# Kernel tuning notes

Hardware: AMD Instinct MI355X
Metric: run time of the kernel (lower is better)

## Reference

```python
import jax, jax.numpy as jnp
import numpy as np

P = 7       # patch (window) size
H_HEADS = 8
D_HEAD = 64
SCALE = D_HEAD ** -0.5


def setup_inputs() -> dict:
    key = jax.random.key(0)
    k1, k2, k3, k4 = jax.random.split(key, 4)
    dim, inner = 256, H_HEADS * D_HEAD
    fmap = jax.random.normal(k1, (32, 56, 56, dim), dtype=jnp.float32)
    Wq = jax.random.normal(k2, (dim, inner), dtype=jnp.float32) * (dim ** -0.5)
    Wkv = jax.random.normal(k3, (dim, 2 * inner), dtype=jnp.float32) * (dim ** -0.5)
    Wo = jax.random.normal(k4, (inner, dim), dtype=jnp.float32) * (inner ** -0.5)
    bo = jnp.zeros((dim,), dtype=jnp.float32)
    return {"fmap": fmap, "Wq": Wq, "Wkv": Wkv, "Wo": Wo, "bo": bo}


def reference(fmap, Wq, Wkv, Wo, bo):
    b, X, Y, c = fmap.shape
    x, y = X // P, Y // P
    h, d = H_HEADS, D_HEAD
    # window partition: b (x p1) (y p2) c -> (b x y) p1 p2 c
    f = fmap.reshape(b, x, P, y, P, c).transpose(0, 1, 3, 2, 4, 5)
    f = f.reshape(b * x * y, P, P, c)
    # 1x1 convs == matmul over channels
    q = f @ Wq                       # (B, p, p, h*d)
    k_, v = jnp.split(f @ Wkv, 2, axis=-1)
    B = b * x * y
    pp = P * P
    def to_heads(t):  # (B,p,p,h*d) -> (B,h,pp,d)
        return t.reshape(B, pp, h, d).transpose(0, 2, 1, 3)
    q, k_, v = map(to_heads, (q, k_, v))
    dots = jnp.einsum('bhid,bhjd->bhij', q, k_) * SCALE
    attn = jax.nn.softmax(dots, axis=-1)
    out = jnp.einsum('bhij,bhjd->bhid', attn, v)      # (B,h,pp,d)
    # (b x y h) (p1 p2) d -> b (x p1) (y p2) (h d)
    out = out.reshape(b, x, y, h, P, P, d)
    out = out.transpose(0, 1, 4, 2, 5, 3, 6).reshape(b, X, Y, h * d)
    return out @ Wo + bo
```

## Files before the change

### kernel.cpp

```cpp
#include <hip/hip_runtime.h>
#include <hip/hip_bf16.h>

typedef __bf16 bf16;
typedef __bf16 bf16x4 __attribute__((ext_vector_type(4)));
typedef __bf16 bf16x8 __attribute__((ext_vector_type(8)));
typedef float f32x4 __attribute__((ext_vector_type(4)));

#define TOK 100352
#define ATT_SCALE 0.125f

#define GLOAD_LDS16(g, l)                                                        \
  __builtin_amdgcn_global_load_lds((const __attribute__((address_space(1))) void*)(g), \
                                   (__attribute__((address_space(3))) void*)(l), 16, 0, 0)

__global__ __launch_bounds__(256) void prep_k(const float* __restrict__ Wq,
                                              const float* __restrict__ Wkv,
                                              const float* __restrict__ Wo,
                                              bf16* __restrict__ Wqkv_t,
                                              bf16* __restrict__ Wo_p) {
  int b = blockIdx.x;
  if (b < 384) {
    __shared__ float t[32][33];
    int bx = b % 48, by = b / 48;
    const float* in;
    bf16* out;
    int C, c0, r0 = by * 32;
    if (bx < 16) { in = Wq; C = 512; c0 = bx * 32; out = Wqkv_t; }
    else { in = Wkv; C = 1024; c0 = (bx - 16) * 32; out = Wqkv_t + 512 * 256; }
    int tx = threadIdx.x & 31, ty = threadIdx.x >> 5;
#pragma unroll
    for (int i = ty; i < 32; i += 8)
      t[i][tx] = in[(size_t)(r0 + i) * C + c0 + tx];
    __syncthreads();
#pragma unroll
    for (int i = ty; i < 32; i += 8)
      out[(size_t)(c0 + i) * 256 + r0 + tx] = (bf16)t[tx][i];
  } else {
    int t = (b - 384) * 256 + threadIdx.x;
    int f = t >> 6, l = t & 63;
    int kk = f & 1, h = (f >> 1) & 7, n = (f >> 4) & 3, wvv = f >> 6;
    int row = wvv * 64 + n * 16 + (l & 15);
    int col = h * 64 + kk * 32 + (l >> 4) * 8;
    bf16x8 o;
#pragma unroll
    for (int e = 0; e < 8; ++e) o[e] = (bf16)Wo[(size_t)(col + e) * 256 + row];
    *(bf16x8*)(Wo_p + (size_t)f * 512 + l * 8) = o;
  }
}

__global__ __launch_bounds__(256) void padzero_k(bf16* __restrict__ Vtg, int nwh) {
  int t = blockIdx.x * 256 + threadIdx.x;
  int wh = t >> 6, dd = t & 63;
  if (wh < nwh) {
    uint4 z = {0, 0, 0, 0};
    char* p = (char*)(Vtg + (size_t)wh * 4096 + dd * 64 + 48);
    *(uint4*)p = z;
    *(uint4*)(p + 16) = z;
  }
}

__global__ __launch_bounds__(256) void qkvg_k(const float* __restrict__ fmap,
                                              const bf16* __restrict__ Bt,
                                              bf16* __restrict__ qkv2,
                                              bf16* __restrict__ Vtg, int wbase0) {
  __shared__ bf16 Bs[2][128 * 64];
  const int tid = threadIdx.x;
  const int lane = tid & 63, wv = tid >> 6;
  const int l15 = lane & 15, l4 = lane >> 4;
  const int g = blockIdx.x;
  const int blk = blockIdx.y;
  bf16x8 af[2][8];
  int wl[2], tt[2];
#pragma unroll
  for (int m = 0; m < 2; ++m) {
    int tokl = blk * 128 + wv * 32 + m * 16 + l15;
    int w = tokl / 49, t = tokl - w * 49;
    wl[m] = w; tt[m] = t;
    int wg = wbase0 + w;
    int p1 = t / 7, p2 = t - p1 * 7;
    const float* ab = fmap +
        (size_t)((((wg >> 6) * 56) + ((wg >> 3) & 7) * 7 + p1) * 56 + (wg & 7) * 7 + p2) * 256;
#pragma unroll
    for (int j = 0; j < 8; ++j) {
      const float* p = ab + j * 32 + l4 * 8;
      float4 f0 = *(const float4*)p;
      float4 f1 = *(const float4*)(p + 4);
      bf16x8 o;
      o[0] = (bf16)f0.x; o[1] = (bf16)f0.y; o[2] = (bf16)f0.z; o[3] = (bf16)f0.w;
      o[4] = (bf16)f1.x; o[5] = (bf16)f1.y; o[6] = (bf16)f1.z; o[7] = (bf16)f1.w;
      af[m][j] = o;
    }
  }
  const int sg = lane >> 3;
  const int scol = ((lane & 7) ^ (sg & 7)) * 8;
#define STAGE_B(tt_, buf_)                                                                   \
  do {                                                                                       \
    int bn_ = g * 4 + ((tt_) >> 2), ks_ = (tt_) & 3;                                         \
    _Pragma("unroll") for (int i_ = 0; i_ < 4; ++i_)                                         \
        GLOAD_LDS16(Bt + (size_t)(bn_ * 128 + wv * 32 + i_ * 8 + sg) * 256 + ks_ * 64 + scol,\
                    Bs[buf_] + wv * 2048 + i_ * 512);                                        \
  } while (0)

  f32x4 acc[2][8] = {};
  STAGE_B(0, 0);
  __syncthreads();
#pragma unroll
  for (int t = 0; t < 16; ++t) {
    const int cur = t & 1, ks = t & 3;
    if (t < 15) STAGE_B(t + 1, cur ^ 1);
#pragma unroll
    for (int kk = 0; kk < 2; ++kk) {
      bf16x8 bfr[8];
#pragma unroll
      for (int n = 0; n < 8; ++n) {
        int rv = n * 16 + l15;
        bfr[n] = *(const bf16x8*)((const char*)Bs[cur] +
                 ((rv * 128 + kk * 64 + l4 * 16) ^ ((rv & 7) << 4)));
      }
#pragma unroll
      for (int m = 0; m < 2; ++m)
#pragma unroll
        for (int n = 0; n < 8; ++n)
          acc[m][n] = __builtin_amdgcn_mfma_f32_16x16x32_bf16(bfr[n], af[m][ks * 2 + kk],
                                                              acc[m][n], 0, 0, 0);
    }
    if (ks == 3) {
      const int bn = g * 4 + (t >> 2);
      if (g < 2) {
#pragma unroll
        for (int m = 0; m < 2; ++m) {
          size_t row = (size_t)blk * 128 + wv * 32 + m * 16 + l15;
#pragma unroll
          for (int n = 0; n < 8; ++n) {
            bf16x4 pk;
#pragma unroll
            for (int r = 0; r < 4; ++r) pk[r] = (bf16)acc[m][n][r];
            *(bf16x4*)(qkv2 + row * 1024 + bn * 128 + n * 16 + l4 * 4) = pk;
          }
        }
      } else {
#pragma unroll
        for (int m = 0; m < 2; ++m) {
#pragma unroll
          for (int n = 0; n < 8; ++n) {
            int d0 = (bn - 8) * 128 + n * 16 + l4 * 4;
            int h = d0 >> 6, dd = d0 & 63;
            size_t vb = ((size_t)wl[m] * 8 + h) * 4096 + (size_t)dd * 64 + tt[m];
#pragma unroll
            for (int r = 0; r < 4; ++r) Vtg[vb + (size_t)r * 64] = (bf16)acc[m][n][r];
          }
        }
      }
#pragma unroll
      for (int m = 0; m < 2; ++m)
#pragma unroll
        for (int n = 0; n < 8; ++n) acc[m][n] = (f32x4){0.f, 0.f, 0.f, 0.f};
    }
    __syncthreads();
  }
#undef STAGE_B
}

__global__ __launch_bounds__(256) void attn2_k(const bf16* __restrict__ qkv2,
                                               const bf16* __restrict__ Vtg,
                                               const bf16* __restrict__ Wo_p,
                                               const float* __restrict__ bias,
                                               float* __restrict__ out, int wbase) {
  __shared__ bf16 Qs[64 * 64], Ks[64 * 64], Vt[64 * 64], Ps[4 * 16 * 64], HO[64 * 64];
  const int w = blockIdx.x;
  const int tid = threadIdx.x, lane = tid & 63, wv = tid >> 6;
  const int l15 = lane & 15, l4 = lane >> 4;
  const size_t bqk = (size_t)w * 49 * 1024;
  const bf16* vbase = Vtg + (size_t)w * 8 * 4096;
  const int wg = wbase + w;
  char* pbase = (char*)Ps + wv * 2048;
  const int sr = wv * 8 + (lane >> 3);
  const int scc = ((lane & 7) ^ ((lane >> 3) & 7)) * 8;
  f32x4 acco[4][4] = {};
  for (int h = 0; h < 8; ++h) {
#pragma unroll
    for (int i = 0; i < 2; ++i) {
      GLOAD_LDS16(qkv2 + bqk + (size_t)(i * 32 + sr) * 1024 + h * 64 + scc,
                  Qs + i * 2048 + wv * 512);
      GLOAD_LDS16(qkv2 + bqk + (size_t)(i * 32 + sr) * 1024 + 512 + h * 64 + scc,
                  Ks + i * 2048 + wv * 512);
      GLOAD_LDS16(vbase + (size_t)h * 4096 + (i * 32 + sr) * 64 + scc,
                  Vt + i * 2048 + wv * 512);
    }
    __syncthreads();
    f32x4 s[4] = {};
#pragma unroll
    for (int kk = 0; kk < 2; ++kk) {
      int rq = wv * 16 + l15;
      bf16x8 aq = *(const bf16x8*)((const char*)Qs +
                  ((rq * 128 + kk * 64 + l4 * 16) ^ ((rq & 7) << 4)));
#pragma unroll
      for (int n = 0; n < 4; ++n) {
        int rk = n * 16 + l15;
        bf16x8 bk = *(const bf16x8*)((const char*)Ks +
                    ((rk * 128 + kk * 64 + l4 * 16) ^ ((rk & 7) << 4)));
        s[n] = __builtin_amdgcn_mfma_f32_16x16x32_bf16(aq, bk, s[n], 0, 0, 0);
      }
    }
    float pr[4][4];
#pragma unroll
    for (int reg = 0; reg < 4; ++reg) {
      float m = -1e30f;
#pragma unroll
      for (int n = 0; n < 4; ++n) {
        float v = s[n][reg] * ATT_SCALE;
        if (n * 16 + l15 < 49) m = fmaxf(m, v);
      }
#pragma unroll
      for (int d = 1; d < 16; d <<= 1) m = fmaxf(m, __shfl_xor(m, d));
      float sum = 0.f;
#pragma unroll
      for (int n = 0; n < 4; ++n) {
        float p = (n * 16 + l15 < 49) ? __expf(s[n][reg] * ATT_SCALE - m) : 0.f;
        pr[n][reg] = p;
        sum += p;
      }
#pragma unroll
      for (int d = 1; d < 16; d <<= 1) sum += __shfl_xor(sum, d);
      float inv = 1.f / sum;
#pragma unroll
      for (int n = 0; n < 4; ++n) pr[n][reg] *= inv;
    }
#pragma unroll
    for (int n = 0; n < 4; ++n)
#pragma unroll
      for (int reg = 0; reg < 4; ++reg) {
        int rl = l4 * 4 + reg, col = n * 16 + l15;
        int off = ((rl * 64 + col) * 2) ^ ((rl & 7) << 4);
        *(bf16*)(pbase + off) = (bf16)pr[n][reg];
      }
    f32x4 o[4] = {};
#pragma unroll
    for (int kk = 0; kk < 2; ++kk) {
      int rp = l15;
      bf16x8 ap = *(const bf16x8*)(pbase +
                  ((rp * 128 + kk * 64 + l4 * 16) ^ ((rp & 7) << 4)));
#pragma unroll
      for (int n = 0; n < 4; ++n) {
        int rv = n * 16 + l15;
        bf16x8 bv = *(const bf16x8*)((const char*)Vt +
                    ((rv * 128 + kk * 64 + l4 * 16) ^ ((rv & 7) << 4)));
        o[n] = __builtin_amdgcn_mfma_f32_16x16x32_bf16(bv, ap, o[n], 0, 0, 0);
      }
    }
    {
      int hrow = wv * 16 + l15;
#pragma unroll
      for (int n = 0; n < 4; ++n) {
        bf16x4 pk;
#pragma unroll
        for (int r = 0; r < 4; ++r) pk[r] = (bf16)o[n][r];
        int off = (hrow * 128 + n * 32 + l4 * 8) ^ ((hrow & 7) << 4);
        *(bf16x4*)((char*)HO + off) = pk;
      }
    }
    __syncthreads();
#pragma unroll
    for (int kk = 0; kk < 2; ++kk) {
      bf16x8 af[4];
#pragma unroll
      for (int m = 0; m < 4; ++m) {
        int r = m * 16 + l15;
        af[m] = *(const bf16x8*)((const char*)HO +
                 ((r * 128 + kk * 64 + l4 * 16) ^ ((r & 7) << 4)));
      }
#pragma unroll
      for (int n = 0; n < 4; ++n) {
        int f = ((wv * 4 + n) * 8 + h) * 2 + kk;
        bf16x8 bv = *(const bf16x8*)(Wo_p + (size_t)f * 512 + lane * 8);
#pragma unroll
        for (int m = 0; m < 4; ++m)
          acco[m][n] = __builtin_amdgcn_mfma_f32_16x16x32_bf16(bv, af[m], acco[m][n], 0, 0, 0);
      }
    }
  }
  int bb = wg >> 6, xx = (wg >> 3) & 7, yy = wg & 7;
#pragma unroll
  for (int m = 0; m < 4; ++m) {
    int rl = m * 16 + l15;
    if (rl < 49) {
      int p1 = rl / 7, p2 = rl - p1 * 7;
      size_t orow = (size_t)(bb * 56 + xx * 7 + p1) * 56 + yy * 7 + p2;
      float* op = out + orow * 256 + wv * 64;
#pragma unroll
      for (int n = 0; n < 4; ++n) {
        int col = n * 16 + l4 * 4;
        float4 b4 = *(const float4*)(bias + wv * 64 + col);
        float4 v;
        v.x = acco[m][n][0] + b4.x;
        v.y = acco[m][n][1] + b4.y;
        v.z = acco[m][n][2] + b4.z;
        v.w = acco[m][n][3] + b4.w;
        *(float4*)(op + col) = v;
      }
    }
  }
}

extern "C" void kernel_launch(void* const* d_in, const int* in_sizes, int n_in,
                              void* d_out, int out_size, void* d_ws, size_t ws_size,
                              hipStream_t stream) {
  const float* fmap = (const float*)d_in[0];
  const float* Wq = (const float*)d_in[1];
  const float* Wkv = (const float*)d_in[2];
  const float* Wo = (const float*)d_in[3];
  const float* bo = (const float*)d_in[4];
  float* out = (float*)d_out;
  char* ws = (char*)d_ws;

  const size_t WQKV_B = 1536ull * 256 * 2;
  const size_t WOP_B = 256ull * 512 * 2;
  const size_t wbytes = WQKV_B + WOP_B;

  int nc = 0;
  size_t Tc = 0, VtgB = 0;
  for (int c = 2; c <= 16; c <<= 1) {
    size_t tc = TOK / c;
    size_t vb = (tc / 49) * 65536ull;
    if (wbytes + vb + tc * 2048ull + 65536ull <= ws_size) { nc = c; Tc = tc; VtgB = vb; break; }
  }
  if (nc == 0) return;

  bf16* Wqkv_t = (bf16*)(ws);
  bf16* Wo_p = (bf16*)(ws + WQKV_B);
  bf16* Vtg = (bf16*)(ws + wbytes);
  bf16* qkv2 = (bf16*)(ws + wbytes + VtgB);

  hipLaunchKernelGGL(prep_k, dim3(448), dim3(256), 0, stream, Wq, Wkv, Wo, Wqkv_t, Wo_p);
  int nwh = (int)(Tc / 49) * 8;
  hipLaunchKernelGGL(padzero_k, dim3((nwh * 64 + 255) / 256), dim3(256), 0, stream, Vtg, nwh);

  for (int c = 0; c < nc; ++c) {
    int tok0 = (int)(c * Tc);
    int wloc = (int)(Tc / 49);
    hipLaunchKernelGGL(qkvg_k, dim3(3, (int)(Tc / 128)), dim3(256), 0, stream, fmap, Wqkv_t,
                       qkv2, Vtg, tok0 / 49);
    hipLaunchKernelGGL(attn2_k, dim3(wloc), dim3(256), 0, stream, qkv2, Vtg, Wo_p, bo, out,
                       tok0 / 49);
  }
}
```

Before: 323.5 us.

## Overlap QKV projection of chunk two with attention of chunk one in fused kernel

After: 443.1 us. +37.0%, slower.

```diff
diff --git a/kernel.cpp b/kernel.cpp
--- a/kernel.cpp
+++ b/kernel.cpp
@@ -59,16 +59,13 @@
   }
 }
 
-__global__ __launch_bounds__(256) void qkvg_k(const float* __restrict__ fmap,
-                                              const bf16* __restrict__ Bt,
-                                              bf16* __restrict__ qkv2,
-                                              bf16* __restrict__ Vtg, int wbase0) {
-  __shared__ bf16 Bs[2][128 * 64];
+__device__ __forceinline__ void qkvg_body(int g, int blk, const float* __restrict__ fmap,
+                                          const bf16* __restrict__ Bt,
+                                          bf16* __restrict__ qkv2, bf16* __restrict__ Vtg,
+                                          int wbase0, bf16* Bs0, bf16* Bs1) {
   const int tid = threadIdx.x;
   const int lane = tid & 63, wv = tid >> 6;
   const int l15 = lane & 15, l4 = lane >> 4;
-  const int g = blockIdx.x;
-  const int blk = blockIdx.y;
   bf16x8 af[2][8];
   int wl[2], tt[2];
 #pragma unroll
@@ -93,28 +90,30 @@
   }
   const int sg = lane >> 3;
   const int scol = ((lane & 7) ^ (sg & 7)) * 8;
-#define STAGE_B(tt_, buf_)                                                                   \
-  do {                                                                                       \
-    int bn_ = g * 4 + ((tt_) >> 2), ks_ = (tt_) & 3;                                         \
-    _Pragma("unroll") for (int i_ = 0; i_ < 4; ++i_)                                         \
-        GLOAD_LDS16(Bt + (size_t)(bn_ * 128 + wv * 32 + i_ * 8 + sg) * 256 + ks_ * 64 + scol,\
-                    Bs[buf_] + wv * 2048 + i_ * 512);                                        \
-  } while (0)
-
+  bf16* Bsp[2] = {Bs0, Bs1};
   f32x4 acc[2][8] = {};
-  STAGE_B(0, 0);
+#pragma unroll
+  for (int i = 0; i < 4; ++i)
+    GLOAD_LDS16(Bt + (size_t)(g * 4 * 128 + wv * 32 + i * 8 + sg) * 256 + scol,
+                Bs0 + wv * 2048 + i * 512);
   __syncthreads();
 #pragma unroll
   for (int t = 0; t < 16; ++t) {
     const int cur = t & 1, ks = t & 3;
-    if (t < 15) STAGE_B(t + 1, cur ^ 1);
+    if (t < 15) {
+      int bn_ = g * 4 + ((t + 1) >> 2), ks_ = (t + 1) & 3;
+#pragma unroll
+      for (int i = 0; i < 4; ++i)
+        GLOAD_LDS16(Bt + (size_t)(bn_ * 128 + wv * 32 + i * 8 + sg) * 256 + ks_ * 64 + scol,
+                    Bsp[cur ^ 1] + wv * 2048 + i * 512);
+    }
 #pragma unroll
     for (int kk = 0; kk < 2; ++kk) {
       bf16x8 bfr[8];
 #pragma unroll
       for (int n = 0; n < 8; ++n) {
         int rv = n * 16 + l15;
-        bfr[n] = *(const bf16x8*)((const char*)Bs[cur] +
+        bfr[n] = *(const bf16x8*)((const char*)Bsp[cur] +
                  ((rv * 128 + kk * 64 + l4 * 16) ^ ((rv & 7) << 4)));
       }
 #pragma unroll
@@ -158,21 +157,19 @@
     }
     __syncthreads();
   }
-#undef STAGE_B
-}
-
-__global__ __launch_bounds__(256) void attn2_k(const bf16* __restrict__ qkv2,
-                                               const bf16* __restrict__ Vtg,
-                                               const bf16* __restrict__ Wo_p,
-                                               const float* __restrict__ bias,
-                                               float* __restrict__ out, int wbase) {
-  __shared__ bf16 Qs[64 * 64], Ks[64 * 64], Vt[64 * 64], Ps[4 * 16 * 64], HO[64 * 64];
-  const int w = blockIdx.x;
+}
+
+__device__ __forceinline__ void attn_body(int win, const bf16* __restrict__ qkv2,
+                                          const bf16* __restrict__ Vtg,
+                                          const bf16* __restrict__ Wo_p,
+                                          const float* __restrict__ bias,
+                                          float* __restrict__ out, int wbase, bf16* Qs,
+                                          bf16* Ks, bf16* Vt, bf16* Ps, bf16* HO) {
   const int tid = threadIdx.x, lane = tid & 63, wv = tid >> 6;
   const int l15 = lane & 15, l4 = lane >> 4;
-  const size_t bqk = (size_t)w * 49 * 1024;
-  const bf16* vbase = Vtg + (size_t)w * 8 * 4096;
-  const int wg = wbase + w;
+  const size_t bqk = (size_t)win * 49 * 1024;
+  const bf16* vbase = Vtg + (size_t)win * 8 * 4096;
+  const int wg = wbase + win;
   char* pbase = (char*)Ps + wv * 2048;
   const int sr = wv * 8 + (lane >> 3);
   const int scc = ((lane & 7) ^ ((lane >> 3) & 7)) * 8;
@@ -205,18 +202,18 @@
     float pr[4][4];
 #pragma unroll
     for (int reg = 0; reg < 4; ++reg) {
-      float m = -1e30f;
+      float mx = -1e30f;
 #pragma unroll
       for (int n = 0; n < 4; ++n) {
         float v = s[n][reg] * ATT_SCALE;
-        if (n * 16 + l15 < 49) m = fmaxf(m, v);
-      }
-#pragma unroll
-      for (int d = 1; d < 16; d <<= 1) m = fmaxf(m, __shfl_xor(m, d));
+        if (n * 16 + l15 < 49) mx = fmaxf(mx, v);
+      }
+#pragma unroll
+      for (int d = 1; d < 16; d <<= 1) mx = fmaxf(mx, __shfl_xor(mx, d));
       float sum = 0.f;
 #pragma unroll
       for (int n = 0; n < 4; ++n) {
-        float p = (n * 16 + l15 < 49) ? __expf(s[n][reg] * ATT_SCALE - m) : 0.f;
+        float p = (n * 16 + l15 < 49) ? __expf(s[n][reg] * ATT_SCALE - mx) : 0.f;
         pr[n][reg] = p;
         sum += p;
       }
@@ -262,11 +259,11 @@
     __syncthreads();
 #pragma unroll
     for (int kk = 0; kk < 2; ++kk) {
-      bf16x8 af[4];
+      bf16x8 afr[4];
 #pragma unroll
       for (int m = 0; m < 4; ++m) {
         int r = m * 16 + l15;
-        af[m] = *(const bf16x8*)((const char*)HO +
+        afr[m] = *(const bf16x8*)((const char*)HO +
                  ((r * 128 + kk * 64 + l4 * 16) ^ ((r & 7) << 4)));
       }
 #pragma unroll
@@ -275,7 +272,7 @@
         bf16x8 bv = *(const bf16x8*)(Wo_p + (size_t)f * 512 + lane * 8);
 #pragma unroll
         for (int m = 0; m < 4; ++m)
-          acco[m][n] = __builtin_amdgcn_mfma_f32_16x16x32_bf16(bv, af[m], acco[m][n], 0, 0, 0);
+          acco[m][n] = __builtin_amdgcn_mfma_f32_16x16x32_bf16(bv, afr[m], acco[m][n], 0, 0, 0);
       }
     }
   }
@@ -299,6 +296,46 @@
         *(float4*)(op + col) = v;
       }
     }
+  }
+}
+
+__global__ __launch_bounds__(256) void qkvg_k(const float* __restrict__ fmap,
+                                              const bf16* __restrict__ Bt,
+                                              bf16* __restrict__ qkv2,
+                                              bf16* __restrict__ Vtg, int wbase0) {
+  __shared__ bf16 Bs[2][128 * 64];
+  qkvg_body(blockIdx.x, blockIdx.y, fmap, Bt, qkv2, Vtg, wbase0, Bs[0], Bs[1]);
+}
+
+__global__ __launch_bounds__(256) void attn2_k(const bf16* __restrict__ qkv2,
+                                               const bf16* __restrict__ Vtg,
+                                               const bf16* __restrict__ Wo_p,
+                                               const float* __restrict__ bias,
+                                               float* __restrict__ out, int wbase) {
+  __shared__ bf16 Qs[64 * 64], Ks[64 * 64], Vt[64 * 64], Ps[4 * 16 * 64], HO[64 * 64];
+  attn_body(blockIdx.x, qkv2, Vtg, Wo_p, bias, out, wbase, Qs, Ks, Vt, Ps, HO);
+}
+
+__global__ __launch_bounds__(256) void fusedmid_k(const float* __restrict__ fmap,
+                                                  const bf16* __restrict__ Bt,
+                                                  bf16* __restrict__ qkv2_p,
+                                                  bf16* __restrict__ Vtg_p, int wbase_p,
+                                                  const bf16* __restrict__ qkv2_c,
+                                                  const bf16* __restrict__ Vtg_c,
+                                                  const bf16* __restrict__ Wo_p,
+                                                  const float* __restrict__ bias,
+                                                  float* __restrict__ out, int wbase_c) {
+  __shared__ char smem[40960];
+  int bx = blockIdx.x;
+  bool is_attn = (bx < 2048) && (bx & 1);
+  if (is_attn) {
+    attn_body(bx >> 1, qkv2_c, Vtg_c, Wo_p, bias, out, wbase_c, (bf16*)smem,
+              (bf16*)(smem + 8192), (bf16*)(smem + 16384), (bf16*)(smem + 24576),
+              (bf16*)(smem + 32768));
+  } else {
+    int qidx = (bx < 2048) ? (bx >> 1) : 1024 + (bx - 2048);
+    qkvg_body(qidx % 3, qidx / 3, fmap, Bt, qkv2_p, Vtg_p, wbase_p, (bf16*)smem,
+              (bf16*)(smem + 16384));
   }
 }
 
@@ -317,30 +354,49 @@
   const size_t WOP_B = 256ull * 512 * 2;
   const size_t wbytes = WQKV_B + WOP_B;
 
-  int nc = 0;
-  size_t Tc = 0, VtgB = 0;
-  for (int c = 2; c <= 16; c <<= 1) {
-    size_t tc = TOK / c;
-    size_t vb = (tc / 49) * 65536ull;
-    if (wbytes + vb + tc * 2048ull + 65536ull <= ws_size) { nc = c; Tc = tc; VtgB = vb; break; }
-  }
-  if (nc == 0) return;
+  const size_t Tc = TOK / 2;
+  const size_t QkvB = Tc * 2048;
+  const size_t VtgB = (Tc / 49) * 65536ull;
+  const size_t needDb = wbytes + 2 * (VtgB + QkvB) + 65536;
 
   bf16* Wqkv_t = (bf16*)(ws);
   bf16* Wo_p = (bf16*)(ws + WQKV_B);
-  bf16* Vtg = (bf16*)(ws + wbytes);
-  bf16* qkv2 = (bf16*)(ws + wbytes + VtgB);
 
   hipLaunchKernelGGL(prep_k, dim3(448), dim3(256), 0, stream, Wq, Wkv, Wo, Wqkv_t, Wo_p);
-  int nwh = (int)(Tc / 49) * 8;
-  hipLaunchKernelGGL(padzero_k, dim3((nwh * 64 + 255) / 256), dim3(256), 0, stream, Vtg, nwh);
-
-  for (int c = 0; c < nc; ++c) {
-    int tok0 = (int)(c * Tc);
-    int wloc = (int)(Tc / 49);
+
+  if (needDb <= ws_size) {
+    bf16* Vtg0 = (bf16*)(ws + wbytes);
+    bf16* Vtg1 = (bf16*)(ws + wbytes + VtgB);
+    bf16* qkv0 = (bf16*)(ws + wbytes + 2 * VtgB);
+    bf16* qkv1 = (bf16*)(ws + wbytes + 2 * VtgB + QkvB);
+    int nwh = (int)(Tc / 49) * 8 * 2;
+    hipLaunchKernelGGL(padzero_k, dim3((nwh * 64 + 255) / 256), dim3(256), 0, stream,
+                       Vtg0, nwh);
     hipLaunchKernelGGL(qkvg_k, dim3(3, (int)(Tc / 128)), dim3(256), 0, stream, fmap, Wqkv_t,
-                       qkv2, Vtg, tok0 / 49);
-    hipLaunchKernelGGL(attn2_k, dim3(wloc), dim3(256), 0, stream, qkv2, Vtg, Wo_p, bo, out,
-                       tok0 / 49);
-  }
-}
+                       qkv0, Vtg0, 0);
+    hipLaunchKernelGGL(fusedmid_k, dim3(2200), dim3(256), 0, stream, fmap, Wqkv_t, qkv1, Vtg1,
+                       1024, qkv0, Vtg0, Wo_p, bo, out, 0);
+    hipLaunchKernelGGL(attn2_k, dim3((int)(Tc / 49)), dim3(256), 0, stream, qkv1, Vtg1, Wo_p,
+                       bo, out, 1024);
+  } else {
+    int nc = 0;
+    size_t tcv = 0, vb = 0;
+    for (int c = 2; c <= 16; c <<= 1) {
+      size_t tc = TOK / c;
+      size_t v = (tc / 49) * 65536ull;
+      if (wbytes + v + tc * 2048ull + 65536ull <= ws_size) { nc = c; tcv = tc; vb = v; break; }
+    }
+    if (nc == 0) return;
+    bf16* Vtg = (bf16*)(ws + wbytes);
+    bf16* qkv2 = (bf16*)(ws + wbytes + vb);
+    int nwh = (int)(tcv / 49) * 8;
+    hipLaunchKernelGGL(padzero_k, dim3((nwh * 64 + 255) / 256), dim3(256), 0, stream, Vtg, nwh);
+    for (int c = 0; c < nc; ++c) {
+      int tok0 = (int)(c * tcv);
+      hipLaunchKernelGGL(qkvg_k, dim3(3, (int)(tcv / 128)), dim3(256), 0, stream, fmap, Wqkv_t,
+                         qkv2, Vtg, tok0 / 49);
+      hipLaunchKernelGGL(attn2_k, dim3((int)(tcv / 49)), dim3(256), 0, stream, qkv2, Vtg, Wo_p,
+                         bo, out, tok0 / 49);
+    }
+  }
+}
```
